# Optimization experiments

Hardware: AMD Instinct MI355X
Metric: run time of the kernel (lower is better)

The kernel has to match this reference:

```python
import jax, jax.numpy as jnp
import numpy as np

K = 4
G = 64
IN_DIM = 256
OUT_DIM = 256
BATCH = 512
T0, T1 = -1.0, 1.0


def setup_inputs() -> dict:
    key = jax.random.key(0)
    kx, kw = jax.random.split(key)
    x = jax.random.uniform(kx, (BATCH, IN_DIM), jnp.float32, T0, T1)
    # xavier_normal_ on [G+K, in, out]: std = sqrt(2 / (fan_in + fan_out)) with fan over last two dims
    std = (2.0 / (IN_DIM + OUT_DIM)) ** 0.5
    w = jax.random.normal(kw, (G + K, IN_DIM, OUT_DIM), jnp.float32) * std
    # knot vector: k-1 repeats of t0, linspace(t0,t1,G+1), k-1 repeats of t1
    t = jnp.concatenate([
        jnp.full((K - 1,), T0, jnp.float32),
        jnp.linspace(T0, T1, G + 1, dtype=jnp.float32),
        jnp.full((K - 1,), T1, jnp.float32),
    ])
    return {"x": x, "w": w, "t": t, "k": K}


def _basis(x, t, k):
    """Cox-de Boor: the k nonzero order-k B-spline basis values at each x.
    Returns (idx, N): idx [..., k] basis indices i-k+1..i, N [..., k] values."""
    n_t = t.shape[0]
    # interval i with t[i] <= x < t[i+1], clipped to the valid span
    i = jnp.clip(jnp.searchsorted(t, x, side='right') - 1, k - 1, n_t - k - 1)
    N = jnp.ones(x.shape + (1,), x.dtype)
    for p in range(1, k):  # static small loop (k=4)
        jj = jnp.arange(1, p + 1)
        left = x[..., None] - t[i[..., None] + 1 - jj]   # [..., p]
        right = t[i[..., None] + jj] - x[..., None]      # [..., p]
        saved = jnp.zeros_like(x)
        vals = []
        for r in range(p):
            d = right[..., r] + left[..., p - 1 - r]      # t[i+r+1] - t[i+r+1-p]
            temp = N[..., r] / d
            vals.append(saved + right[..., r] * temp)
            saved = left[..., p - 1 - r] * temp
        vals.append(saved)
        N = jnp.stack(vals, -1)
    idx = i[..., None] - (k - 1) + jnp.arange(k)
    return idx, N


def reference(x, w, t, k):
    in_dim = x.shape[1]
    n_rows = w.shape[0]
    idx, y1 = _basis(x, t, k)                             # [B,in,k], [B,in,k]
    # last row of w (index -1 == n_rows-1) weights the SiLU residual term
    idx_full = jnp.concatenate(
        [idx, jnp.full(idx.shape[:-1] + (1,), n_rows - 1, idx.dtype)], -1)  # [B,in,k+1]
    silu = x * jax.nn.sigmoid(x)
    y2 = jnp.concatenate([y1, silu[..., None]], -1)       # [B,in,k+1]
    # gather local spline coefficients: w2[b,c,j,o] = w[idx_full[b,c,j], c, o]
    w2 = w[idx_full, jnp.arange(in_dim)[None, :, None], :]  # [B,in,k+1,out]
    return jnp.einsum('bcjo,bcj->bo', w2, y2)             # [B,out]
```

## Files before the change

kernel.cpp:

```cpp
#include <hip/hip_runtime.h>
#include <hip/hip_fp16.h>
#include <math.h>
#include <stdint.h>

#define IN_DIM  256
#define OUT_DIM 256
#define NROWS   68
#define NT      71
#define BATCH   512
#define KPAD    96
#define NCG     32
#define PART_FLOATS (NCG * BATCH * OUT_DIM)
#define WB_SHORTS   (IN_DIM * OUT_DIM * KPAD)

typedef _Float16 f16x8 __attribute__((ext_vector_type(8)));
typedef float    f32x4 __attribute__((ext_vector_type(4)));

__global__ __launch_bounds__(256) void cvt_kernel(const float* __restrict__ w,
                                                  unsigned short* __restrict__ wb) {
  __shared__ unsigned short l16[NROWS][264];
  const int c = blockIdx.x;
  const int t = threadIdx.x;
  const int o4 = (t & 63) * 4;
  for (int k = (t >> 6); k < NROWS; k += 4) {
    const float4 v = *(const float4*)(w + ((size_t)k * IN_DIM + c) * OUT_DIM + o4);
    l16[k][o4 + 0] = __half_as_ushort(__float2half_rn(v.x));
    l16[k][o4 + 1] = __half_as_ushort(__float2half_rn(v.y));
    l16[k][o4 + 2] = __half_as_ushort(__float2half_rn(v.z));
    l16[k][o4 + 3] = __half_as_ushort(__float2half_rn(v.w));
  }
  __syncthreads();
  #pragma unroll
  for (int i = 0; i < 12; ++i) {
    const int idx = t + 256 * i;
    const int kb  = idx >> 10;
    const int o   = (idx >> 2) & 255;
    const int g   = idx & 3;
    const int k8  = kb * 32 + g * 8;
    uint32_t hl[4];
    #pragma unroll
    for (int j = 0; j < 4; ++j) {
      const int ka = k8 + 2 * j, k2 = ka + 1;
      const uint32_t lo = (ka < NROWS) ? (uint32_t)l16[ka][o] : 0u;
      const uint32_t hi = (k2 < NROWS) ? (uint32_t)l16[k2][o] : 0u;
      hl[j] = lo | (hi << 16);
    }
    *(uint4*)(wb + (((size_t)(c * 3 + kb) * 256 + o) * 32 + g * 8)) =
        make_uint4(hl[0], hl[1], hl[2], hl[3]);
  }
}

__global__ __launch_bounds__(512) void kan_gather_kernel(
    const float* __restrict__ x, const unsigned short* __restrict__ wbu,
    const float* __restrict__ t, float* __restrict__ part) {
  __shared__ float  lt[NT];
  __shared__ uint4  YldsRaw[832];
  __shared__ float4 nA[8][64];
  __shared__ float  sA[8][64];
  __shared__ int    bA[8][64];
  __shared__ float  bounce[64 * 260];

  unsigned short* Ylds = (unsigned short*)YldsRaw;
  const int tid   = threadIdx.x;
  const int cg    = blockIdx.x & 31;
  const int btile = blockIdx.x >> 5;
  const int wv    = tid >> 6;
  const int lane  = tid & 63;
  const int m16   = lane & 15;
  const int g     = lane >> 4;
  const int ob    = wv * 32;

  if (tid < NT) lt[tid] = t[tid];
  for (int i = tid; i < 832; i += 512)
    YldsRaw[i] = make_uint4(0u, 0u, 0u, 0u);
  __syncthreads();

  {
    const int c = tid >> 6, bb = tid & 63;
    const float xv = x[(size_t)(btile * 64 + bb) * IN_DIM + cg * 8 + c];
    int i = 3 + (int)floorf((xv + 1.0f) * 32.0f);
    i = i < 3 ? 3 : (i > 66 ? 66 : i);
    while (i > 3 && xv < lt[i]) --i;
    while (i < 66 && xv >= lt[i + 1]) ++i;
    float N0 = 1.f, N1 = 0.f, N2 = 0.f, N3 = 0.f;
    { const float l1 = xv - lt[i], r1 = lt[i + 1] - xv;
      const float tp = N0 / (r1 + l1); N1 = l1 * tp; N0 = r1 * tp; }
    { const float l1 = xv - lt[i], l2 = xv - lt[i - 1];
      const float r1 = lt[i + 1] - xv, r2 = lt[i + 2] - xv;
      float saved = 0.f;
      const float tp0 = N0 / (r1 + l2); const float n0 = saved + r1 * tp0; saved = l2 * tp0;
      const float tp1 = N1 / (r2 + l1); const float n1 = saved + r2 * tp1; saved = l1 * tp1;
      N0 = n0; N1 = n1; N2 = saved; }
    { const float l1 = xv - lt[i], l2 = xv - lt[i - 1], l3 = xv - lt[i - 2];
      const float r1 = lt[i + 1] - xv, r2 = lt[i + 2] - xv, r3 = lt[i + 3] - xv;
      float saved = 0.f;
      const float tp0 = N0 / (r1 + l3); const float n0 = saved + r1 * tp0; saved = l3 * tp0;
      const float tp1 = N1 / (r2 + l2); const float n1 = saved + r2 * tp1; saved = l2 * tp1;
      const float tp2 = N2 / (r3 + l1); const float n2 = saved + r3 * tp2; saved = l1 * tp2;
      N0 = n0; N1 = n1; N2 = n2; N3 = saved; }
    nA[c][bb] = make_float4(N0, N1, N2, N3);
    sA[c][bb] = xv / (1.0f + expf(-xv));
    bA[c][bb] = i - 3;
  }
  __syncthreads();

  const uint4* wbu4 = (const uint4*)wbu;
  f32x4 acc[2][4];
  #pragma unroll
  for (int ot = 0; ot < 2; ++ot)
    #pragma unroll
    for (int bt = 0; bt < 4; ++bt) acc[ot][bt] = f32x4{0.f, 0.f, 0.f, 0.f};

  int prevb = -1;
  for (int ch = 0; ch < 8; ++ch) {
    if (tid < 64) {
      unsigned short* yr = Ylds + tid * 104;
      if (prevb >= 0) {
        yr[prevb + 0] = 0; yr[prevb + 1] = 0; yr[prevb + 2] = 0; yr[prevb + 3] = 0;
      }
      const float4 yv = nA[ch][tid];
      const int base = bA[ch][tid];
      yr[base + 0] = __half_as_ushort(__float2half_rn(yv.x));
      yr[base + 1] = __half_as_ushort(__float2half_rn(yv.y));
      yr[base + 2] = __half_as_ushort(__float2half_rn(yv.z));
      yr[base + 3] = __half_as_ushort(__float2half_rn(yv.w));
      yr[67]       = __half_as_ushort(__float2half_rn(sA[ch][tid]));
      prevb = base;
    }
    uint4 af[6];
    {
      const int c3 = (cg * 8 + ch) * 3;
      #pragma unroll
      for (int ot = 0; ot < 2; ++ot)
        #pragma unroll
        for (int kb = 0; kb < 3; ++kb)
          af[ot * 3 + kb] =
              wbu4[((size_t)(c3 + kb) * 256 + ob + ot * 16 + m16) * 4 + g];
    }
    __syncthreads();

    #pragma unroll
    for (int kb = 0; kb < 3; ++kb) {
      #pragma unroll
      for (int bt = 0; bt < 4; ++bt) {
        const f16x8 bf = *(const f16x8*)(Ylds + (bt * 16 + m16) * 104 + kb * 32 + g * 8);
        acc[0][bt] = __builtin_amdgcn_mfma_f32_16x16x32_f16(
            __builtin_bit_cast(f16x8, af[0 * 3 + kb]), bf, acc[0][bt], 0, 0, 0);
        acc[1][bt] = __builtin_amdgcn_mfma_f32_16x16x32_f16(
            __builtin_bit_cast(f16x8, af[1 * 3 + kb]), bf, acc[1][bt], 0, 0, 0);
      }
    }
    __syncthreads();
  }

  #pragma unroll
  for (int ot = 0; ot < 2; ++ot)
    #pragma unroll
    for (int bt = 0; bt < 4; ++bt)
      #pragma unroll
      for (int r = 0; r < 4; ++r)
        bounce[(bt * 16 + m16) * 260 + ob + ot * 16 + g * 4 + r] = acc[ot][bt][r];
  __syncthreads();
  #pragma unroll
  for (int i = 0; i < 8; ++i) {
    const int idx = tid + 512 * i;
    const int b = idx >> 6, o4 = (idx & 63) * 4;
    *(float4*)(part + ((size_t)cg * BATCH + btile * 64 + b) * OUT_DIM + o4) =
        *(const float4*)(bounce + b * 260 + o4);
  }
}

__global__ __launch_bounds__(256) void reduce_kernel(const float* __restrict__ part,
                                                     float* __restrict__ out) {
  const int q = blockIdx.x * 256 + threadIdx.x;
  const int S = BATCH * OUT_DIM / 4;
  const float4* p = (const float4*)part;
  float4 s = p[q];
  #pragma unroll
  for (int k = 1; k < NCG; ++k) {
    const float4 a = p[q + k * S];
    s.x += a.x; s.y += a.y; s.z += a.z; s.w += a.w;
  }
  ((float4*)out)[q] = s;
}

extern "C" void kernel_launch(void* const* d_in, const int* in_sizes, int n_in,
                              void* d_out, int out_size, void* d_ws, size_t ws_size,
                              hipStream_t stream) {
  const float* x = (const float*)d_in[0];
  const float* w = (const float*)d_in[1];
  const float* t = (const float*)d_in[2];
  float* out  = (float*)d_out;
  float* part = (float*)d_ws;
  unsigned short* wb = (unsigned short*)((float*)d_ws + PART_FLOATS);
  cvt_kernel<<<IN_DIM, 256, 0, stream>>>(w, wb);
  kan_gather_kernel<<<256, 512, 0, stream>>>(x, wb, t, part);
  reduce_kernel<<<BATCH * OUT_DIM / 4 / 256, 256, 0, stream>>>(part, out);
}
```

Before: 96.99 us.

## Materialize full 8-channel sparse basis tile in LDS and drop per-channel barriers

Each thread now writes its fp16 basis values and SiLU term directly into one LDS tile holding all 8 channels (pitch 776 halfs per batch row), instead of staging the results and re-scattering them channel by channel from a single thread group. The MFMA loop then runs over 24 K-blocks without the two __syncthreads per channel, and the same LDS buffer is reused for the output bounce. This removes the serialized 64-thread scatter phase and 16 barriers, at the cost of a larger zero-initialized LDS tile and loads issued inside the unrolled loop without explicit double buffering.

```diff
diff --git a/kernel.cpp b/kernel.cpp
--- a/kernel.cpp
+++ b/kernel.cpp
@@ -10,6 +10,7 @@
 #define BATCH   512
 #define KPAD    96
 #define NCG     32
+#define PITCH   776
 #define PART_FLOATS (NCG * BATCH * OUT_DIM)
 #define WB_SHORTS   (IN_DIM * OUT_DIM * KPAD)
 
@@ -53,14 +54,11 @@
 __global__ __launch_bounds__(512) void kan_gather_kernel(
     const float* __restrict__ x, const unsigned short* __restrict__ wbu,
     const float* __restrict__ t, float* __restrict__ part) {
-  __shared__ float  lt[NT];
-  __shared__ uint4  YldsRaw[832];
-  __shared__ float4 nA[8][64];
-  __shared__ float  sA[8][64];
-  __shared__ int    bA[8][64];
-  __shared__ float  bounce[64 * 260];
+  __shared__ float lt[NT];
+  __shared__ char  smem[64 * PITCH * 2];
 
-  unsigned short* Ylds = (unsigned short*)YldsRaw;
+  unsigned short* Y = (unsigned short*)smem;
+  float* bounce = (float*)smem;
   const int tid   = threadIdx.x;
   const int cg    = blockIdx.x & 31;
   const int btile = blockIdx.x >> 5;
@@ -71,8 +69,11 @@
   const int ob    = wv * 32;
 
   if (tid < NT) lt[tid] = t[tid];
-  for (int i = tid; i < 832; i += 512)
-    YldsRaw[i] = make_uint4(0u, 0u, 0u, 0u);
+  {
+    uint4* y4 = (uint4*)smem;
+    for (int i = tid; i < 64 * PITCH / 8; i += 512)
+      y4[i] = make_uint4(0u, 0u, 0u, 0u);
+  }
   __syncthreads();
 
   {
@@ -98,9 +99,13 @@
       const float tp1 = N1 / (r2 + l2); const float n1 = saved + r2 * tp1; saved = l2 * tp1;
       const float tp2 = N2 / (r3 + l1); const float n2 = saved + r3 * tp2; saved = l1 * tp2;
       N0 = n0; N1 = n1; N2 = n2; N3 = saved; }
-    nA[c][bb] = make_float4(N0, N1, N2, N3);
-    sA[c][bb] = xv / (1.0f + expf(-xv));
-    bA[c][bb] = i - 3;
+    unsigned short* yr = Y + (size_t)bb * PITCH + c * KPAD;
+    const int base = i - 3;
+    yr[base + 0] = __half_as_ushort(__float2half_rn(N0));
+    yr[base + 1] = __half_as_ushort(__float2half_rn(N1));
+    yr[base + 2] = __half_as_ushort(__float2half_rn(N2));
+    yr[base + 3] = __half_as_ushort(__float2half_rn(N3));
+    yr[67]       = __half_as_ushort(__float2half_rn(xv / (1.0f + expf(-xv))));
   }
   __syncthreads();
 
@@ -111,47 +116,21 @@
     #pragma unroll
     for (int bt = 0; bt < 4; ++bt) acc[ot][bt] = f32x4{0.f, 0.f, 0.f, 0.f};
 
-  int prevb = -1;
-  for (int ch = 0; ch < 8; ++ch) {
-    if (tid < 64) {
-      unsigned short* yr = Ylds + tid * 104;
-      if (prevb >= 0) {
-        yr[prevb + 0] = 0; yr[prevb + 1] = 0; yr[prevb + 2] = 0; yr[prevb + 3] = 0;
-      }
-      const float4 yv = nA[ch][tid];
-      const int base = bA[ch][tid];
-      yr[base + 0] = __half_as_ushort(__float2half_rn(yv.x));
-      yr[base + 1] = __half_as_ushort(__float2half_rn(yv.y));
-      yr[base + 2] = __half_as_ushort(__float2half_rn(yv.z));
-      yr[base + 3] = __half_as_ushort(__float2half_rn(yv.w));
-      yr[67]       = __half_as_ushort(__float2half_rn(sA[ch][tid]));
-      prevb = base;
+  #pragma unroll 8
+  for (int j = 0; j < 24; ++j) {
+    const size_t rowb = ((size_t)(cg * 24 + j)) * 256;
+    const uint4 af0 = wbu4[(rowb + ob + m16) * 4 + g];
+    const uint4 af1 = wbu4[(rowb + ob + 16 + m16) * 4 + g];
+    #pragma unroll
+    for (int bt = 0; bt < 4; ++bt) {
+      const f16x8 bf = *(const f16x8*)(Y + (size_t)(bt * 16 + m16) * PITCH + j * 32 + g * 8);
+      acc[0][bt] = __builtin_amdgcn_mfma_f32_16x16x32_f16(
+          __builtin_bit_cast(f16x8, af0), bf, acc[0][bt], 0, 0, 0);
+      acc[1][bt] = __builtin_amdgcn_mfma_f32_16x16x32_f16(
+          __builtin_bit_cast(f16x8, af1), bf, acc[1][bt], 0, 0, 0);
     }
-    uint4 af[6];
-    {
-      const int c3 = (cg * 8 + ch) * 3;
-      #pragma unroll
-      for (int ot = 0; ot < 2; ++ot)
-        #pragma unroll
-        for (int kb = 0; kb < 3; ++kb)
-          af[ot * 3 + kb] =
-              wbu4[((size_t)(c3 + kb) * 256 + ob + ot * 16 + m16) * 4 + g];
-    }
-    __syncthreads();
-
-    #pragma unroll
-    for (int kb = 0; kb < 3; ++kb) {
-      #pragma unroll
-      for (int bt = 0; bt < 4; ++bt) {
-        const f16x8 bf = *(const f16x8*)(Ylds + (bt * 16 + m16) * 104 + kb * 32 + g * 8);
-        acc[0][bt] = __builtin_amdgcn_mfma_f32_16x16x32_f16(
-            __builtin_bit_cast(f16x8, af[0 * 3 + kb]), bf, acc[0][bt], 0, 0, 0);
-        acc[1][bt] = __builtin_amdgcn_mfma_f32_16x16x32_f16(
-            __builtin_bit_cast(f16x8, af[1 * 3 + kb]), bf, acc[1][bt], 0, 0, 0);
-      }
-    }
-    __syncthreads();
   }
+  __syncthreads();
 
   #pragma unroll
   for (int ot = 0; ot < 2; ++ot)
```

Result: no change. 97.28 us (+0.3%).
